# Kernel optimization log

Hardware: AMD Instinct MI355X
Metric: run time of the kernel (lower is better)

The kernel has to match this reference:

```python
import jax, jax.numpy as jnp
import numpy as np

D = 512; NH = 8; FF = 2048; LE = 6; LD = 6; V = 97; SM = 512; SQ = 128; B = 16
EPS = 1e-5


def _posenc(length, depth):
    half = depth // 2
    pos = jnp.arange(length, dtype=jnp.float32)[:, None]
    dep = jnp.arange(half, dtype=jnp.float32)[None, :] / half
    ang = pos / (10000.0 ** dep)
    return jnp.concatenate([jnp.sin(ang), jnp.cos(ang)], axis=-1)  # [length, depth]


def _ln(x, w, b):
    mu = jnp.mean(x, axis=-1, keepdims=True)
    var = jnp.mean((x - mu) ** 2, axis=-1, keepdims=True)
    return (x - mu) * jax.lax.rsqrt(var + EPS) * w + b


def _heads(t, S, Bt):
    return t.reshape(S, Bt * NH, D // NH).transpose(1, 0, 2)  # [B*H, S, dk]


def _self_attn(x, wqkv, bqkv, wo, bo, causal):
    S, Bt, _ = x.shape
    qkv = x @ wqkv.T + bqkv
    q, k, v = jnp.split(qkv, 3, axis=-1)
    q = _heads(q, S, Bt); k = _heads(k, S, Bt); v = _heads(v, S, Bt)
    scores = jnp.einsum('hqd,hkd->hqk', q, k) / jnp.sqrt(jnp.asarray(D // NH, x.dtype))
    if causal:
        mask = jnp.triu(jnp.ones((S, S), bool), 1)
        scores = jnp.where(mask[None], -jnp.inf, scores)
    attn = jax.nn.softmax(scores, axis=-1)
    out = jnp.einsum('hqk,hkd->hqd', attn, v).transpose(1, 0, 2).reshape(S, Bt, D)
    return out @ wo.T + bo


def _cross_attn(query, memory, wq, bq, wk, bk, wv, bv, wo, bo):
    Sq, Bt, _ = query.shape
    Sm = memory.shape[0]
    q = _heads(query @ wq.T + bq, Sq, Bt)
    k = _heads(memory @ wk.T + bk, Sm, Bt)
    v = _heads(memory @ wv.T + bv, Sm, Bt)
    scores = jnp.einsum('hqd,hkd->hqk', q, k) / jnp.sqrt(jnp.asarray(D // NH, query.dtype))
    attn = jax.nn.softmax(scores, axis=-1)
    out = jnp.einsum('hqk,hkd->hqd', attn, v).transpose(1, 0, 2).reshape(Sq, Bt, D)
    return out @ wo.T + bo


def _forward(src, tokens, tok_emb,
             enc_qkv_w, enc_qkv_b, enc_out_w, enc_out_b,
             enc_l1_w, enc_l1_b, enc_l2_w, enc_l2_b,
             enc_n1_w, enc_n1_b, enc_n2_w, enc_n2_b,
             dec_qkv_w, dec_qkv_b, dec_sout_w, dec_sout_b,
             dec_q_w, dec_q_b, dec_k_w, dec_k_b, dec_v_w, dec_v_b,
             dec_cout_w, dec_cout_b,
             dec_l1_w, dec_l1_b, dec_l2_w, dec_l2_b,
             dec_n1_w, dec_n1_b, dec_n2_w, dec_n2_b, dec_n3_w, dec_n3_b,
             out_w, out_b):
    # ---- encoder ----
    x = src  # [SM, B, D]
    for i in range(LE):
        x2 = _self_attn(x, enc_qkv_w[i], enc_qkv_b[i], enc_out_w[i], enc_out_b[i], causal=False)
        x = _ln(x + x2, enc_n1_w[i], enc_n1_b[i])
        x2 = jax.nn.relu(x @ enc_l1_w[i].T + enc_l1_b[i]) @ enc_l2_w[i].T + enc_l2_b[i]
        x = _ln(x + x2, enc_n2_w[i], enc_n2_b[i])
    memory = x
    # ---- decoder ----
    tgt = tok_emb[tokens] + _posenc(tokens.shape[0], D)[:, None, :]  # [SQ, B, D]
    for i in range(LD):
        x2 = _self_attn(tgt, dec_qkv_w[i], dec_qkv_b[i], dec_sout_w[i], dec_sout_b[i], causal=True)
        tgt = _ln(tgt + x2, dec_n1_w[i], dec_n1_b[i])
        x2 = _cross_attn(tgt, memory, dec_q_w[i], dec_q_b[i], dec_k_w[i], dec_k_b[i],
                         dec_v_w[i], dec_v_b[i], dec_cout_w[i], dec_cout_b[i])
        tgt = _ln(tgt + x2, dec_n2_w[i], dec_n2_b[i])
        x2 = jax.nn.relu(tgt @ dec_l1_w[i].T + dec_l1_b[i]) @ dec_l2_w[i].T + dec_l2_b[i]
        tgt = _ln(tgt + x2, dec_n3_w[i], dec_n3_b[i])
    return tgt @ out_w.T + out_b  # [SQ, B, V]


def setup_inputs() -> dict:
    key = jax.random.key(0)
    ks = iter(jax.random.split(key, 64))
    g = lambda shape: jax.random.normal(next(ks), shape, dtype=jnp.float32) * 0.02
    inp = {
        'src': jax.random.normal(next(ks), (SM, B, D), dtype=jnp.float32),
        'tokens': jax.random.randint(next(ks), (SQ, B), 0, V),
        'tok_emb': g((V, D)),
        'enc_qkv_w': g((LE, 3 * D, D)), 'enc_qkv_b': g((LE, 3 * D)),
        'enc_out_w': g((LE, D, D)), 'enc_out_b': g((LE, D)),
        'enc_l1_w': g((LE, FF, D)), 'enc_l1_b': g((LE, FF)),
        'enc_l2_w': g((LE, D, FF)), 'enc_l2_b': g((LE, D)),
        'enc_n1_w': jnp.ones((LE, D)), 'enc_n1_b': jnp.zeros((LE, D)),
        'enc_n2_w': jnp.ones((LE, D)), 'enc_n2_b': jnp.zeros((LE, D)),
        'dec_qkv_w': g((LD, 3 * D, D)), 'dec_qkv_b': g((LD, 3 * D)),
        'dec_sout_w': g((LD, D, D)), 'dec_sout_b': g((LD, D)),
        'dec_q_w': g((LD, D, D)), 'dec_q_b': g((LD, D)),
        'dec_k_w': g((LD, D, D)), 'dec_k_b': g((LD, D)),
        'dec_v_w': g((LD, D, D)), 'dec_v_b': g((LD, D)),
        'dec_cout_w': g((LD, D, D)), 'dec_cout_b': g((LD, D)),
        'dec_l1_w': g((LD, FF, D)), 'dec_l1_b': g((LD, FF)),
        'dec_l2_w': g((LD, D, FF)), 'dec_l2_b': g((LD, D)),
        'dec_n1_w': jnp.ones((LD, D)), 'dec_n1_b': jnp.zeros((LD, D)),
        'dec_n2_w': jnp.ones((LD, D)), 'dec_n2_b': jnp.zeros((LD, D)),
        'dec_n3_w': jnp.ones((LD, D)), 'dec_n3_b': jnp.zeros((LD, D)),
        'out_w': g((V, D)), 'out_b': g((V,)),
    }
    return inp


def reference(src, tokens, tok_emb,
              enc_qkv_w, enc_qkv_b, enc_out_w, enc_out_b,
              enc_l1_w, enc_l1_b, enc_l2_w, enc_l2_b,
              enc_n1_w, enc_n1_b, enc_n2_w, enc_n2_b,
              dec_qkv_w, dec_qkv_b, dec_sout_w, dec_sout_b,
              dec_q_w, dec_q_b, dec_k_w, dec_k_b, dec_v_w, dec_v_b,
              dec_cout_w, dec_cout_b,
              dec_l1_w, dec_l1_b, dec_l2_w, dec_l2_b,
              dec_n1_w, dec_n1_b, dec_n2_w, dec_n2_b, dec_n3_w, dec_n3_b,
              out_w, out_b):
    return _forward(src, tokens, tok_emb,
                    enc_qkv_w, enc_qkv_b, enc_out_w, enc_out_b,
                    enc_l1_w, enc_l1_b, enc_l2_w, enc_l2_b,
                    enc_n1_w, enc_n1_b, enc_n2_w, enc_n2_b,
                    dec_qkv_w, dec_qkv_b, dec_sout_w, dec_sout_b,
                    dec_q_w, dec_q_b, dec_k_w, dec_k_b, dec_v_w, dec_v_b,
                    dec_cout_w, dec_cout_b,
                    dec_l1_w, dec_l1_b, dec_l2_w, dec_l2_b,
                    dec_n1_w, dec_n1_b, dec_n2_w, dec_n2_b, dec_n3_w, dec_n3_b,
                    out_w, out_b)
```

## Files before the change

### kernel.cpp

```cpp
#include <hip/hip_runtime.h>
#include <hip/hip_bf16.h>
#include <cstddef>
#include <cstdint>

#define D_MODEL 512
#define BATCH 16
#define EPS_LN 1e-5f

typedef __bf16 bf16x8 __attribute__((ext_vector_type(8)));
typedef float f32x4 __attribute__((ext_vector_type(4)));
typedef unsigned short u16x8 __attribute__((ext_vector_type(8)));
typedef unsigned short u16x4 __attribute__((ext_vector_type(4)));
typedef unsigned short u16x2 __attribute__((ext_vector_type(2)));

__device__ __forceinline__ void gload_lds16(const void* g, void* l) {
    __builtin_amdgcn_global_load_lds(
        (const __attribute__((address_space(1))) void*)g,
        (__attribute__((address_space(3))) void*)l,
        16, 0, 0);
}

template <int BM, int OUTBF16, int SWAP>
__global__ __launch_bounds__(256) void gemm_mfma(
    const __bf16* __restrict__ A, const __bf16* __restrict__ W,
    const __bf16* __restrict__ W2, int wsplit,
    const float* __restrict__ bias, const float* __restrict__ bias2, int bsplit,
    void* __restrict__ Cout, __bf16* __restrict__ VTout, int m_vt0, int log2S,
    int N, int Mlim, int MS, int K, int relu, int permrow)
{
    constexpr int WC     = (BM == 128) ? 2 : 4;
    constexpr int WSPAN  = 128 / WC;
    constexpr int NC     = WSPAN / 16;
    constexpr int ABYTES = BM * 128;
    constexpr int PA     = ABYTES / 4096;
    constexpr int BUFB   = ABYTES + 16384;

    __shared__ __align__(16) char smem[2 * BUFB];

    const int tid  = threadIdx.x;
    const int lane = tid & 63;
    const int wid  = tid >> 6;
    const int wrow = (BM == 128) ? (wid >> 1) : 0;
    const int wcol = (BM == 128) ? (wid & 1) : wid;
    const int row0 = blockIdx.y * BM;
    const int col0 = blockIdx.x * 128;

    const int lrow  = lane & 15;
    const int lhalf = lane >> 4;
    const int koff0 = ((lhalf) ^ (lrow & 7)) * 16;
    const int koff1 = ((4 + lhalf) ^ (lrow & 7)) * 16;

    const int srow = tid >> 3;
    const int slot = tid & 7;
    const int sg   = slot ^ (srow & 7);

    f32x4 acc[4][NC] = {};

    const __bf16* Wsel = W;
    int wc0 = col0;
    if (col0 >= wsplit) { Wsel = W2; wc0 = col0 - wsplit; }

    const __bf16* Abase = A + (size_t)(row0 + srow) * K + sg * 8;
    const __bf16* Wbase = Wsel + (size_t)(wc0 + srow) * K + sg * 8;

    auto stage = [&](char* buf, int kt) {
#pragma unroll
        for (int p = 0; p < PA; ++p)
            gload_lds16(Abase + (size_t)p * 32 * K + kt, buf + p * 4096 + tid * 16);
#pragma unroll
        for (int p = 0; p < 4; ++p)
            gload_lds16(Wbase + (size_t)p * 32 * K + kt,
                        buf + ABYTES + p * 4096 + tid * 16);
    };

    stage(smem, 0);
    const int nkt = K >> 6;
    int cur = 0;
    for (int kt = 0; kt < nkt; ++kt) {
        __syncthreads();
        if (kt + 1 < nkt) stage(smem + (cur ^ 1) * BUFB, (kt + 1) * 64);
        const char* aB = smem + cur * BUFB + (wrow * 64 + lrow) * 128;
        const char* wB = smem + cur * BUFB + ABYTES + (wcol * WSPAN + lrow) * 128;
#pragma unroll
        for (int ks = 0; ks < 2; ++ks) {
            const int ko = ks ? koff1 : koff0;
            bf16x8 af[4], bfr[NC];
#pragma unroll
            for (int m = 0; m < 4; ++m) af[m]  = *(const bf16x8*)(aB + m * 2048 + ko);
#pragma unroll
            for (int n = 0; n < NC; ++n) bfr[n] = *(const bf16x8*)(wB + n * 2048 + ko);
            if (SWAP) {
#pragma unroll
                for (int m = 0; m < 4; ++m)
#pragma unroll
                    for (int n = 0; n < NC; ++n)
                        acc[m][n] = __builtin_amdgcn_mfma_f32_16x16x32_bf16(
                            bfr[n], af[m], acc[m][n], 0, 0, 0);
            } else {
#pragma unroll
                for (int m = 0; m < 4; ++m)
#pragma unroll
                    for (int n = 0; n < NC; ++n)
                        acc[m][n] = __builtin_amdgcn_mfma_f32_16x16x32_bf16(
                            af[m], bfr[n], acc[m][n], 0, 0, 0);
            }
        }
        cur ^= 1;
    }

    if (SWAP) {
#pragma unroll
        for (int m = 0; m < 4; ++m) {
            const int r = row0 + wrow * 64 + m * 16 + lrow;
#pragma unroll
            for (int n = 0; n < NC; ++n) {
                const int c0 = col0 + wcol * WSPAN + n * 16 + lhalf * 4;
                const float4 bv = *(const float4*)(bias + c0);
                float o0 = acc[m][n][0] + bv.x, o1 = acc[m][n][1] + bv.y;
                float o2 = acc[m][n][2] + bv.z, o3 = acc[m][n][3] + bv.w;
                if (relu) {
                    o0 = fmaxf(o0, 0.f); o1 = fmaxf(o1, 0.f);
                    o2 = fmaxf(o2, 0.f); o3 = fmaxf(o3, 0.f);
                }
                if (OUTBF16) {
                    union { __bf16 h4[4]; u16x4 u; } pk;
                    pk.h4[0] = (__bf16)o0; pk.h4[1] = (__bf16)o1;
                    pk.h4[2] = (__bf16)o2; pk.h4[3] = (__bf16)o3;
                    *(u16x4*)((__bf16*)Cout + (size_t)r * MS + c0) = pk.u;
                } else {
                    *(float4*)((float*)Cout + (size_t)r * MS + c0) =
                        make_float4(o0, o1, o2, o3);
                }
            }
        }
    } else {
        const int orow = row0 + wrow * 64 + lhalf * 4;
        const int ocol = col0 + wcol * WSPAN + lrow;
        const int smask = (1 << log2S) - 1;
#pragma unroll
        for (int n = 0; n < NC; ++n) {
            const int c = ocol + n * 16;
            if (c >= m_vt0) {
                const int cv = c - m_vt0;
                const int hh = cv >> 6, dd = cv & 63;
                const float bv = (bias2 && c >= bsplit) ? bias2[c - bsplit] : bias[c];
#pragma unroll
                for (int m = 0; m < 4; ++m) {
                    const int rr = orow + m * 16;
                    const int bb = rr >> log2S, ss = rr & smask;
                    union { __bf16 h4[4]; u16x4 u; } pk;
#pragma unroll
                    for (int j = 0; j < 4; ++j)
                        pk.h4[j] = (__bf16)(acc[m][n][j] + bv);
                    *(u16x4*)(VTout + (((size_t)((bb * 8 + hh) * 64 + dd)) << log2S) + ss) = pk.u;
                }
            } else if (c < Mlim) {
                const float bv = (bias2 && c >= bsplit) ? bias2[c - bsplit] : bias[c];
#pragma unroll
                for (int m = 0; m < 4; ++m) {
#pragma unroll
                    for (int j = 0; j < 4; ++j) {
                        int rr = orow + m * 16 + j;
                        if (permrow) rr = ((rr & smask) * BATCH) + (rr >> log2S);
                        float v = acc[m][n][j] + bv;
                        if (relu) v = fmaxf(v, 0.f);
                        if (OUTBF16) ((__bf16*)Cout)[(size_t)rr * MS + c] = (__bf16)v;
                        else         ((float*)Cout)[(size_t)rr * MS + c] = v;
                    }
                }
            }
        }
    }
}

template <int CAUSAL>
__global__ __launch_bounds__(256) void attn_mfma(
    const __bf16* __restrict__ Qb, const __bf16* __restrict__ Kb,
    const __bf16* __restrict__ VT, __bf16* __restrict__ Op,
    int Sq, int Skv, int qstride, int kstride, int koff, float scale)
{
    __shared__ __align__(16) char smem[40960];
    const int tid = threadIdx.x;
    const int l   = tid & 63;
    const int w   = tid >> 6;
    char* Psm = smem + 32768 + w * 2048;

    const int qc = blockIdx.x;
    const int h  = blockIdx.y;
    const int b  = blockIdx.z;
    const int l15 = l & 15;
    const int g   = l >> 4;
    const int sw  = l15 & 7;

    const int sq = qc * 64 + w * 16 + l15;
    const __bf16* qrow = Qb + ((size_t)(b * Sq + sq)) * qstride + h * 64 + g * 8;
    const bf16x8 qf0 = *(const bf16x8*)(qrow);
    const bf16x8 qf1 = *(const bf16x8*)(qrow + 32);

    const int srow = tid >> 3;
    const int slot = tid & 7;

    auto stageKV = [&](char* buf, int kc) {
#pragma unroll
        for (int p = 0; p < 2; ++p) {
            const int r   = p * 32 + srow;
            const int sgo = (slot ^ (r & 7)) * 8;
            const __bf16* ksrc = Kb + ((size_t)(b * Skv + kc * 64 + r)) * kstride
                                    + koff + h * 64 + sgo;
            gload_lds16(ksrc, buf + (p * 256 + tid) * 16);
            const __bf16* vsrc = VT + ((size_t)((b * 8 + h) * 64 + r)) * Skv
                                    + kc * 64 + sgo;
            gload_lds16(vsrc, buf + 8192 + (p * 256 + tid) * 16);
        }
    };

    f32x4 acc[4] = {};
    float m_run = -1e30f, l_run = 0.f;

    const int nkc = CAUSAL ? (qc + 1) : (Skv >> 6);
    stageKV(smem, 0);
    int cur = 0;
    for (int kc = 0; kc < nkc; ++kc) {
        __syncthreads();
        if (kc + 1 < nkc) stageKV(smem + (cur ^ 1) * 16384, kc + 1);
        const char* Ksm = smem + cur * 16384;
        const char* Vsm = Ksm + 8192;

        f32x4 st[4];
#pragma unroll
        for (int f = 0; f < 4; ++f) {
            const char* kr = Ksm + (f * 16 + l15) * 128;
            bf16x8 ka0 = *(const bf16x8*)(kr + ((g ^ sw) * 16));
            bf16x8 ka1 = *(const bf16x8*)(kr + (((4 + g) ^ sw) * 16));
            f32x4 z = {};
            z = __builtin_amdgcn_mfma_f32_16x16x32_bf16(ka0, qf0, z, 0, 0, 0);
            st[f] = __builtin_amdgcn_mfma_f32_16x16x32_bf16(ka1, qf1, z, 0, 0, 0);
        }

        float rmax = -1e30f;
#pragma unroll
        for (int f = 0; f < 4; ++f)
#pragma unroll
            for (int j = 0; j < 4; ++j) {
                float v = st[f][j] * scale;
                if (CAUSAL) {
                    if (kc * 64 + f * 16 + g * 4 + j > sq) v = -1e30f;
                }
                st[f][j] = v;
                rmax = fmaxf(rmax, v);
            }
        rmax = fmaxf(rmax, __shfl_xor(rmax, 16, 64));
        rmax = fmaxf(rmax, __shfl_xor(rmax, 32, 64));
        const float mn = fmaxf(m_run, rmax);
        const float corr = __expf(m_run - mn);
        m_run = mn;
        float rsum = 0.f;
#pragma unroll
        for (int f = 0; f < 4; ++f)
#pragma unroll
            for (int j = 0; j < 4; ++j) {
                float p = __expf(st[f][j] - mn);
                st[f][j] = p;
                rsum += p;
            }
        rsum += __shfl_xor(rsum, 16, 64);
        rsum += __shfl_xor(rsum, 32, 64);
        l_run = l_run * corr + rsum;

#pragma unroll
        for (int j = 0; j < 4; ++j) {
            const float cj = __shfl(corr, g * 20 + j, 64);
            acc[0][j] *= cj; acc[1][j] *= cj; acc[2][j] *= cj; acc[3][j] *= cj;
        }

#pragma unroll
        for (int f = 0; f < 4; ++f)
#pragma unroll
            for (int j2 = 0; j2 < 2; ++j2) {
                union { __bf16 h2[2]; unsigned u; } cv;
                cv.h2[0] = (__bf16)st[f][2 * j2];
                cv.h2[1] = (__bf16)st[f][2 * j2 + 1];
                const int key0 = 16 * f + 4 * g + 2 * j2;
                const int byte = l15 * 128 + (((key0 >> 3) ^ sw) * 16) + (key0 & 7) * 2;
                *(unsigned*)(Psm + byte) = cv.u;
            }

#pragma unroll
        for (int ks = 0; ks < 2; ++ks) {
            const int so = ((4 * ks + g) ^ sw) * 16;
            bf16x8 pa = *(const bf16x8*)(Psm + l15 * 128 + so);
#pragma unroll
            for (int n = 0; n < 4; ++n) {
                bf16x8 vb = *(const bf16x8*)(Vsm + (n * 16 + l15) * 128 + so);
                acc[n] = __builtin_amdgcn_mfma_f32_16x16x32_bf16(pa, vb, acc[n], 0, 0, 0);
            }
        }
        cur ^= 1;
    }

    const float inv = 1.f / l_run;
#pragma unroll
    for (int j = 0; j < 4; ++j) {
        const float ij = __shfl(inv, g * 20 + j, 64);
        const int s = qc * 64 + w * 16 + g * 4 + j;
        __bf16* orow = Op + ((size_t)(b * Sq + s)) * D_MODEL + h * 64 + l15;
#pragma unroll
        for (int n = 0; n < 4; ++n)
            orow[n * 16] = (__bf16)(acc[n][j] * ij);
    }
}

__global__ __launch_bounds__(256) void add_ln(
    const float* __restrict__ X, const __bf16* __restrict__ Y,
    const float* __restrict__ w, const float* __restrict__ bias,
    float* __restrict__ Of, __bf16* __restrict__ Oh)
{
    const int t   = blockIdx.x;
    const int tid = threadIdx.x;
    const float2 x2 = *(const float2*)(X + (size_t)t * D_MODEL + tid * 2);
    const u16x2 yv = *(const u16x2*)(Y + (size_t)t * D_MODEL + tid * 2);
    union { u16x2 u; __bf16 h2[2]; } yc; yc.u = yv;
    float v0 = x2.x + (float)yc.h2[0], v1 = x2.y + (float)yc.h2[1];
    float sum = v0 + v1;
    float sq  = v0 * v0 + v1 * v1;
#pragma unroll
    for (int off = 32; off; off >>= 1) {
        sum += __shfl_xor(sum, off);
        sq  += __shfl_xor(sq, off);
    }
    __shared__ float ssum[4], ssq[4];
    const int wid = tid >> 6;
    if ((tid & 63) == 0) { ssum[wid] = sum; ssq[wid] = sq; }
    __syncthreads();
    sum = ssum[0] + ssum[1] + ssum[2] + ssum[3];
    sq  = ssq[0] + ssq[1] + ssq[2] + ssq[3];

    const float mu  = sum * (1.f / D_MODEL);
    const float var = sq * (1.f / D_MODEL) - mu * mu;
    const float rs  = rsqrtf(var + EPS_LN);
    const float2 w2 = *(const float2*)(w + tid * 2);
    const float2 b2 = *(const float2*)(bias + tid * 2);
    float o0 = (v0 - mu) * rs * w2.x + b2.x;
    float o1 = (v1 - mu) * rs * w2.y + b2.y;
    *(float2*)(Of + (size_t)t * D_MODEL + tid * 2) = make_float2(o0, o1);
    union { __bf16 h2[2]; u16x2 u; } cv;
    cv.h2[0] = (__bf16)o0; cv.h2[1] = (__bf16)o1;
    *(u16x2*)(Oh + (size_t)t * D_MODEL + tid * 2) = cv.u;
}

__global__ __launch_bounds__(256) void permute_src(
    const float* __restrict__ src, float* __restrict__ Of, __bf16* __restrict__ Oh)
{
    const int t = blockIdx.x;
    const int b = t >> 9, s = t & 511;
    const int tid = threadIdx.x;
    const float2 v = *(const float2*)(src + ((size_t)(s * BATCH + b)) * D_MODEL + tid * 2);
    *(float2*)(Of + (size_t)t * D_MODEL + tid * 2) = v;
    union { __bf16 h2[2]; u16x2 u; } cv;
    cv.h2[0] = (__bf16)v.x; cv.h2[1] = (__bf16)v.y;
    *(u16x2*)(Oh + (size_t)t * D_MODEL + tid * 2) = cv.u;
}

__global__ __launch_bounds__(256) void embed_pos(
    const int* __restrict__ tokens, const float* __restrict__ emb,
    float* __restrict__ Of, __bf16* __restrict__ Oh)
{
    const int t   = blockIdx.x;
    const int b   = t >> 7, s = t & 127;
    const int tid = threadIdx.x;
    const int tok = tokens[s * BATCH + b];
    const float C = 9.210340371976184f / 256.f;
    const int d = tid * 2;
    const int j = (d < 256) ? d : (d - 256);
    float a0 = (float)s * expf(-(float)j * C);
    float a1 = (float)s * expf(-(float)(j + 1) * C);
    float pe0 = (d < 256) ? sinf(a0) : cosf(a0);
    float pe1 = (d < 256) ? sinf(a1) : cosf(a1);
    const float2 e2 = *(const float2*)(emb + (size_t)tok * D_MODEL + d);
    float o0 = e2.x + pe0, o1 = e2.y + pe1;
    *(float2*)(Of + (size_t)t * D_MODEL + d) = make_float2(o0, o1);
    union { __bf16 h2[2]; u16x2 u; } cv;
    cv.h2[0] = (__bf16)o0; cv.h2[1] = (__bf16)o1;
    *(u16x2*)(Oh + (size_t)t * D_MODEL + d) = cv.u;
}

struct CvtSeg { const float* s; __bf16* d; int n8; };
struct CvtArgs { CvtSeg seg[12]; int tot8; };

__global__ __launch_bounds__(256) void cvt_multi(CvtArgs a)
{
    const int stride = gridDim.x * 256;
    for (int u = blockIdx.x * 256 + threadIdx.x; u < a.tot8; u += stride) {
        int v = u;
        for (int sgi = 0; sgi < 12; ++sgi) {
            const int n8 = a.seg[sgi].n8;
            if (v < n8) {
                const float4 f0 = ((const float4*)a.seg[sgi].s)[v * 2];
                const float4 f1 = ((const float4*)a.seg[sgi].s)[v * 2 + 1];
                union { __bf16 h[8]; u16x8 u; } c;
                c.h[0] = (__bf16)f0.x; c.h[1] = (__bf16)f0.y;
                c.h[2] = (__bf16)f0.z; c.h[3] = (__bf16)f0.w;
                c.h[4] = (__bf16)f1.x; c.h[5] = (__bf16)f1.y;
                c.h[6] = (__bf16)f1.z; c.h[7] = (__bf16)f1.w;
                ((u16x8*)a.seg[sgi].d)[v] = c.u;
                break;
            }
            v -= n8;
        }
    }
}

__global__ __launch_bounds__(256) void pad_outw(
    const float* __restrict__ w, __bf16* __restrict__ o)
{
    const int idx = blockIdx.x * 256 + threadIdx.x;
    const int r = idx >> 9;
    const int c = idx & 511;
    o[idx] = (__bf16)(r < 97 ? w[r * 512 + c] : 0.f);
}

extern "C" void kernel_launch(void* const* d_in, const int* in_sizes, int n_in,
                              void* d_out, int out_size, void* d_ws, size_t ws_size,
                              hipStream_t stream)
{
    const float* src     = (const float*)d_in[0];
    const int*   tokens  = (const int*)d_in[1];
    const float* tok_emb = (const float*)d_in[2];
    const float* enc_qkv_w = (const float*)d_in[3];
    const float* enc_qkv_b = (const float*)d_in[4];
    const float* enc_out_w = (const float*)d_in[5];
    const float* enc_out_b = (const float*)d_in[6];
    const float* enc_l1_w  = (const float*)d_in[7];
    const float* enc_l1_b  = (const float*)d_in[8];
    const float* enc_l2_w  = (const float*)d_in[9];
    const float* enc_l2_b  = (const float*)d_in[10];
    const float* enc_n1_w  = (const float*)d_in[11];
    const float* enc_n1_b  = (const float*)d_in[12];
    const float* enc_n2_w  = (const float*)d_in[13];
    const float* enc_n2_b  = (const float*)d_in[14];
    const float* dec_qkv_w = (const float*)d_in[15];
    const float* dec_qkv_b = (const float*)d_in[16];
    const float* dec_sout_w = (const float*)d_in[17];
    const float* dec_sout_b = (const float*)d_in[18];
    const float* dec_q_w   = (const float*)d_in[19];
    const float* dec_q_b   = (const float*)d_in[20];
    const float* dec_k_w   = (const float*)d_in[21];
    const float* dec_k_b   = (const float*)d_in[22];
    const float* dec_v_w   = (const float*)d_in[23];
    const float* dec_v_b   = (const float*)d_in[24];
    const float* dec_cout_w = (const float*)d_in[25];
    const float* dec_cout_b = (const float*)d_in[26];
    const float* dec_l1_w  = (const float*)d_in[27];
    const float* dec_l1_b  = (const float*)d_in[28];
    const float* dec_l2_w  = (const float*)d_in[29];
    const float* dec_l2_b  = (const float*)d_in[30];
    const float* dec_n1_w  = (const float*)d_in[31];
    const float* dec_n1_b  = (const float*)d_in[32];
    const float* dec_n2_w  = (const float*)d_in[33];
    const float* dec_n2_b  = (const float*)d_in[34];
    const float* dec_n3_w  = (const float*)d_in[35];
    const float* dec_n3_b  = (const float*)d_in[36];
    const float* out_w     = (const float*)d_in[37];
    const float* out_b     = (const float*)d_in[38];

    const int NE = 512 * BATCH;
    const int ND = 128 * BATCH;
    const float scale = 0.125f;
    const int BIG = 1 << 30;

    char* w8 = (char*)d_ws;
    float*  Ax_f = (float*) (w8 + 0);
    float*  T_f  = (float*) (w8 + 16777216);
    __bf16* Ax_h = (__bf16*)(w8 + 20971520);
    __bf16* T_h  = (__bf16*)(w8 + 29360128);
    __bf16* AO_h = (__bf16*)(w8 + 31457280);
    __bf16* Y_h  = (__bf16*)(w8 + 39845888);
    __bf16* VT   = (__bf16*)(w8 + 48234496);
    __bf16* OWp  = (__bf16*)(w8 + 56623104);
    char*   Gb   = w8 + 56754176;
    __bf16* Gqk  = (__bf16*)Gb;
    __bf16* Gh   = (__bf16*)Gb;
    __bf16* Gq   = (__bf16*)Gb;
    __bf16* Gk   = (__bf16*)(Gb + 2097152);
    __bf16* WB   = (__bf16*)(w8 + 90308608);

    const bool upfront = ws_size >= (size_t)178388992;

    auto gemmS = [&](const __bf16* Am, const __bf16* Wm, const float* bv,
                     void* C, int N, int M, int K, int relu) {
        const int nb128 = (M / 128) * (N / 128);
        if (nb128 >= 256) {
            dim3 grid(M / 128, N / 128);
            gemm_mfma<128, 1, 1><<<grid, 256, 0, stream>>>(
                Am, Wm, nullptr, BIG, bv, nullptr, 0, C, nullptr, BIG, 0,
                N, M, M, K, relu, 0);
        } else {
            dim3 grid(M / 128, N / 64);
            gemm_mfma<64, 1, 1><<<grid, 256, 0, stream>>>(
                Am, Wm, nullptr, BIG, bv, nullptr, 0, C, nullptr, BIG, 0,
                N, M, M, K, relu, 0);
        }
    };
    auto gemmN = [&](const __bf16* Am, const __bf16* Wm, const __bf16* W2m, int wsplit,
                     const float* bv, const float* bv2, int bsplit,
                     void* C, __bf16* VTp, int m_vt0, int log2S,
                     int N, int M, int MS, int K, bool outbf, int permrow) {
        const int nb128 = ((M + 127) / 128) * (N / 128);
        if (nb128 >= 256) {
            dim3 grid((M + 127) / 128, N / 128);
            if (outbf) gemm_mfma<128, 1, 0><<<grid, 256, 0, stream>>>(
                Am, Wm, W2m, wsplit, bv, bv2, bsplit, C, VTp, m_vt0, log2S,
                N, M, MS, K, 0, permrow);
            else       gemm_mfma<128, 0, 0><<<grid, 256, 0, stream>>>(
                Am, Wm, W2m, wsplit, bv, bv2, bsplit, C, VTp, m_vt0, log2S,
                N, M, MS, K, 0, permrow);
        } else {
            dim3 grid((M + 127) / 128, N / 64);
            if (outbf) gemm_mfma<64, 1, 0><<<grid, 256, 0, stream>>>(
                Am, Wm, W2m, wsplit, bv, bv2, bsplit, C, VTp, m_vt0, log2S,
                N, M, MS, K, 0, permrow);
            else       gemm_mfma<64, 0, 0><<<grid, 256, 0, stream>>>(
                Am, Wm, W2m, wsplit, bv, bv2, bsplit, C, VTp, m_vt0, log2S,
                N, M, MS, K, 0, permrow);
        }
    };
    auto cvt = [&](CvtArgs& a, int blocks) {
        int tot = 0;
        for (int i = 0; i < 12; ++i) tot += a.seg[i].n8;
        a.tot8 = tot;
        cvt_multi<<<blocks, 256, 0, stream>>>(a);
    };

    permute_src<<<NE, 256, 0, stream>>>(src, Ax_f, Ax_h);
    pad_outw<<<256, 256, 0, stream>>>(out_w, OWp);

    __bf16* WencQKV = WB;
    __bf16* WencOUT = WencQKV + 4718592;
    __bf16* WencL1  = WencOUT + 1572864;
    __bf16* WencL2  = WencL1 + 6291456;
    __bf16* WdecQKV = WencL2 + 6291456;
    __bf16* WdecSOUT = WdecQKV + 4718592;
    __bf16* WdecQ   = WdecSOUT + 1572864;
    __bf16* WdecK   = WdecQ + 1572864;
    __bf16* WdecV   = WdecK + 1572864;
    __bf16* WdecCOUT = WdecV + 1572864;
    __bf16* WdecL1  = WdecCOUT + 1572864;
    __bf16* WdecL2  = WdecL1 + 6291456;

    if (upfront) {
        CvtArgs a = {};
        a.seg[0]  = { enc_qkv_w,  WencQKV,  4718592 / 8 };
        a.seg[1]  = { enc_out_w,  WencOUT,  1572864 / 8 };
        a.seg[2]  = { enc_l1_w,   WencL1,   6291456 / 8 };
        a.seg[3]  = { enc_l2_w,   WencL2,   6291456 / 8 };
        a.seg[4]  = { dec_qkv_w,  WdecQKV,  4718592 / 8 };
        a.seg[5]  = { dec_sout_w, WdecSOUT, 1572864 / 8 };
        a.seg[6]  = { dec_q_w,    WdecQ,    1572864 / 8 };
        a.seg[7]  = { dec_k_w,    WdecK,    1572864 / 8 };
        a.seg[8]  = { dec_v_w,    WdecV,    1572864 / 8 };
        a.seg[9]  = { dec_cout_w, WdecCOUT, 1572864 / 8 };
        a.seg[10] = { dec_l1_w,   WdecL1,   6291456 / 8 };
        a.seg[11] = { dec_l2_w,   WdecL2,   6291456 / 8 };
        cvt(a, 2048);
    }

    for (int i = 0; i < 6; ++i) {
        __bf16 *wqkv, *wout, *wl1, *wl2;
        if (upfront) {
            wqkv = WencQKV + (size_t)i * 786432;
            wout = WencOUT + (size_t)i * 262144;
            wl1  = WencL1 + (size_t)i * 1048576;
            wl2  = WencL2 + (size_t)i * 1048576;
        } else {
            wqkv = WB; wout = WB + 786432; wl1 = WB + 1048576; wl2 = WB + 2097152;
            CvtArgs a = {};
            a.seg[0] = { enc_qkv_w + (size_t)i * 786432,  wqkv, 786432 / 8 };
            a.seg[1] = { enc_out_w + (size_t)i * 262144,  wout, 262144 / 8 };
            a.seg[2] = { enc_l1_w  + (size_t)i * 1048576, wl1, 1048576 / 8 };
            a.seg[3] = { enc_l2_w  + (size_t)i * 1048576, wl2, 1048576 / 8 };
            cvt(a, 1024);
        }

        gemmN(Ax_h, wqkv, nullptr, BIG, enc_qkv_b + (size_t)i * 1536, nullptr, 0,
              Gqk, VT, 1024, 9, NE, 1536, 1024, 512, true, 0);
        attn_mfma<0><<<dim3(8, 8, BATCH), 256, 0, stream>>>(
            Gqk, Gqk, VT, AO_h, 512, 512, 1024, 1024, 512, scale);
        gemmS(AO_h, wout, enc_out_b + (size_t)i * 512, Y_h, NE, 512, 512, 0);
        add_ln<<<NE, 256, 0, stream>>>(Ax_f, Y_h,
                                       enc_n1_w + (size_t)i * 512, enc_n1_b + (size_t)i * 512,
                                       Ax_f, Ax_h);
        gemmS(Ax_h, wl1, enc_l1_b + (size_t)i * 2048, Gh, NE, 2048, 512, 1);
        gemmS(Gh, wl2, enc_l2_b + (size_t)i * 512, Y_h, NE, 512, 2048, 0);
        add_ln<<<NE, 256, 0, stream>>>(Ax_f, Y_h,
                                       enc_n2_w + (size_t)i * 512, enc_n2_b + (size_t)i * 512,
                                       Ax_f, Ax_h);
    }

    embed_pos<<<ND, 256, 0, stream>>>(tokens, tok_emb, T_f, T_h);
    for (int i = 0; i < 6; ++i) {
        __bf16 *dqkv, *dsout, *dq, *dk, *dv, *dcout, *dl1, *dl2;
        if (upfront) {
            dqkv  = WdecQKV + (size_t)i * 786432;
            dsout = WdecSOUT + (size_t)i * 262144;
            dq    = WdecQ + (size_t)i * 262144;
            dk    = WdecK + (size_t)i * 262144;
            dv    = WdecV + (size_t)i * 262144;
            dcout = WdecCOUT + (size_t)i * 262144;
            dl1   = WdecL1 + (size_t)i * 1048576;
            dl2   = WdecL2 + (size_t)i * 1048576;
        } else {
            dqkv = WB; dsout = WB + 786432; dq = WB + 1048576; dk = WB + 1310720;
            dv = WB + 1572864; dcout = WB + 1835008; dl1 = WB + 2097152; dl2 = WB + 3145728;
            CvtArgs a = {};
            a.seg[0] = { dec_qkv_w  + (size_t)i * 786432,  dqkv,  786432 / 8 };
            a.seg[1] = { dec_sout_w + (size_t)i * 262144,  dsout, 262144 / 8 };
            a.seg[2] = { dec_q_w    + (size_t)i * 262144,  dq,    262144 / 8 };
            a.seg[3] = { dec_k_w    + (size_t)i * 262144,  dk,    262144 / 8 };
            a.seg[4] = { dec_v_w    + (size_t)i * 262144,  dv,    262144 / 8 };
            a.seg[5] = { dec_cout_w + (size_t)i * 262144,  dcout, 262144 / 8 };
            a.seg[6] = { dec_l1_w   + (size_t)i * 1048576, dl1,  1048576 / 8 };
            a.seg[7] = { dec_l2_w   + (size_t)i * 1048576, dl2,  1048576 / 8 };
            cvt(a, 1024);
        }

        gemmN(T_h, dqkv, nullptr, BIG, dec_qkv_b + (size_t)i * 1536, nullptr, 0,
              Gqk, VT, 1024, 7, ND, 1536, 1024, 512, true, 0);
        attn_mfma<1><<<dim3(2, 8, BATCH), 256, 0, stream>>>(
            Gqk, Gqk, VT, AO_h, 128, 128, 1024, 1024, 512, scale);
        gemmS(AO_h, dsout, dec_sout_b + (size_t)i * 512, Y_h, ND, 512, 512, 0);
        add_ln<<<ND, 256, 0, stream>>>(T_f, Y_h,
                                       dec_n1_w + (size_t)i * 512, dec_n1_b + (size_t)i * 512,
                                       T_f, T_h);
        gemmS(T_h, dq, dec_q_b + (size_t)i * 512, Gq, ND, 512, 512, 0);
        gemmN(Ax_h, dk, dv, 512, dec_k_b + (size_t)i * 512, dec_v_b + (size_t)i * 512, 512,
              Gk, VT, 512, 9, NE, 1024, 512, 512, true, 0);
        attn_mfma<0><<<dim3(2, 8, BATCH), 256, 0, stream>>>(
            Gq, Gk, VT, AO_h, 128, 512, 512, 512, 0, scale);
        gemmS(AO_h, dcout, dec_cout_b + (size_t)i * 512, Y_h, ND, 512, 512, 0);
        add_ln<<<ND, 256, 0, stream>>>(T_f, Y_h,
                                       dec_n2_w + (size_t)i * 512, dec_n2_b + (size_t)i * 512,
                                       T_f, T_h);
        gemmS(T_h, dl1, dec_l1_b + (size_t)i * 2048, Gh, ND, 2048, 512, 1);
        gemmS(Gh, dl2, dec_l2_b + (size_t)i * 512, Y_h, ND, 512, 2048, 0);
        add_ln<<<ND, 256, 0, stream>>>(T_f, Y_h,
                                       dec_n3_w + (size_t)i * 512, dec_n3_b + (size_t)i * 512,
                                       T_f, T_h);
    }

    gemmN(T_h, OWp, nullptr, BIG, out_b, nullptr, 0,
          (float*)d_out, nullptr, BIG, 7, ND, 97, 97, 512, false, 1);
}
```

Measured before the change: 1.652 ms.

## Use 512-thread GEMM blocks with 8 waves and simplify weight conversion segment lookup

```diff
diff --git a/kernel.cpp b/kernel.cpp
--- a/kernel.cpp
+++ b/kernel.cpp
@@ -21,18 +21,17 @@
 }
 
 template <int BM, int OUTBF16, int SWAP>
-__global__ __launch_bounds__(256) void gemm_mfma(
+__global__ __launch_bounds__(512) void gemm_mfma(
     const __bf16* __restrict__ A, const __bf16* __restrict__ W,
     const __bf16* __restrict__ W2, int wsplit,
     const float* __restrict__ bias, const float* __restrict__ bias2, int bsplit,
     void* __restrict__ Cout, __bf16* __restrict__ VTout, int m_vt0, int log2S,
     int N, int Mlim, int MS, int K, int relu, int permrow)
 {
-    constexpr int WC     = (BM == 128) ? 2 : 4;
-    constexpr int WSPAN  = 128 / WC;
-    constexpr int NC     = WSPAN / 16;
+    constexpr int MR     = BM / 32;
+    constexpr int WRSPAN = BM / 2;
     constexpr int ABYTES = BM * 128;
-    constexpr int PA     = ABYTES / 4096;
+    constexpr int PA     = ABYTES / 8192;
     constexpr int BUFB   = ABYTES + 16384;
 
     __shared__ __align__(16) char smem[2 * BUFB];
@@ -40,8 +39,8 @@
     const int tid  = threadIdx.x;
     const int lane = tid & 63;
     const int wid  = tid >> 6;
-    const int wrow = (BM == 128) ? (wid >> 1) : 0;
-    const int wcol = (BM == 128) ? (wid & 1) : wid;
+    const int wrow = wid >> 2;
+    const int wcol = wid & 3;
     const int row0 = blockIdx.y * BM;
     const int col0 = blockIdx.x * 128;
 
@@ -54,7 +53,7 @@
     const int slot = tid & 7;
     const int sg   = slot ^ (srow & 7);
 
-    f32x4 acc[4][NC] = {};
+    f32x4 acc[MR][2] = {};
 
     const __bf16* Wsel = W;
     int wc0 = col0;
@@ -66,11 +65,11 @@
     auto stage = [&](char* buf, int kt) {
 #pragma unroll
         for (int p = 0; p < PA; ++p)
-            gload_lds16(Abase + (size_t)p * 32 * K + kt, buf + p * 4096 + tid * 16);
-#pragma unroll
-        for (int p = 0; p < 4; ++p)
-            gload_lds16(Wbase + (size_t)p * 32 * K + kt,
-                        buf + ABYTES + p * 4096 + tid * 16);
+            gload_lds16(Abase + (size_t)p * 64 * K + kt, buf + p * 8192 + tid * 16);
+#pragma unroll
+        for (int p = 0; p < 2; ++p)
+            gload_lds16(Wbase + (size_t)p * 64 * K + kt,
+                        buf + ABYTES + p * 8192 + tid * 16);
     };
 
     stage(smem, 0);
@@ -79,28 +78,28 @@
     for (int kt = 0; kt < nkt; ++kt) {
         __syncthreads();
         if (kt + 1 < nkt) stage(smem + (cur ^ 1) * BUFB, (kt + 1) * 64);
-        const char* aB = smem + cur * BUFB + (wrow * 64 + lrow) * 128;
-        const char* wB = smem + cur * BUFB + ABYTES + (wcol * WSPAN + lrow) * 128;
+        const char* aB = smem + cur * BUFB + (wrow * WRSPAN + lrow) * 128;
+        const char* wB = smem + cur * BUFB + ABYTES + (wcol * 32 + lrow) * 128;
 #pragma unroll
         for (int ks = 0; ks < 2; ++ks) {
             const int ko = ks ? koff1 : koff0;
-            bf16x8 af[4], bfr[NC];
-#pragma unroll
-            for (int m = 0; m < 4; ++m) af[m]  = *(const bf16x8*)(aB + m * 2048 + ko);
-#pragma unroll
-            for (int n = 0; n < NC; ++n) bfr[n] = *(const bf16x8*)(wB + n * 2048 + ko);
+            bf16x8 af[MR], bfr[2];
+#pragma unroll
+            for (int m = 0; m < MR; ++m) af[m]  = *(const bf16x8*)(aB + m * 2048 + ko);
+#pragma unroll
+            for (int n = 0; n < 2; ++n)  bfr[n] = *(const bf16x8*)(wB + n * 2048 + ko);
             if (SWAP) {
 #pragma unroll
-                for (int m = 0; m < 4; ++m)
-#pragma unroll
-                    for (int n = 0; n < NC; ++n)
+                for (int m = 0; m < MR; ++m)
+#pragma unroll
+                    for (int n = 0; n < 2; ++n)
                         acc[m][n] = __builtin_amdgcn_mfma_f32_16x16x32_bf16(
                             bfr[n], af[m], acc[m][n], 0, 0, 0);
             } else {
 #pragma unroll
-                for (int m = 0; m < 4; ++m)
-#pragma unroll
-                    for (int n = 0; n < NC; ++n)
+                for (int m = 0; m < MR; ++m)
+#pragma unroll
+                    for (int n = 0; n < 2; ++n)
                         acc[m][n] = __builtin_amdgcn_mfma_f32_16x16x32_bf16(
                             af[m], bfr[n], acc[m][n], 0, 0, 0);
             }
@@ -110,11 +109,11 @@
 
     if (SWAP) {
 #pragma unroll
-        for (int m = 0; m < 4; ++m) {
-            const int r = row0 + wrow * 64 + m * 16 + lrow;
-#pragma unroll
-            for (int n = 0; n < NC; ++n) {
-                const int c0 = col0 + wcol * WSPAN + n * 16 + lhalf * 4;
+        for (int m = 0; m < MR; ++m) {
+            const int r = row0 + wrow * WRSPAN + m * 16 + lrow;
+#pragma unroll
+            for (int n = 0; n < 2; ++n) {
+                const int c0 = col0 + wcol * 32 + n * 16 + lhalf * 4;
                 const float4 bv = *(const float4*)(bias + c0);
                 float o0 = acc[m][n][0] + bv.x, o1 = acc[m][n][1] + bv.y;
                 float o2 = acc[m][n][2] + bv.z, o3 = acc[m][n][3] + bv.w;
@@ -134,18 +133,18 @@
             }
         }
     } else {
-        const int orow = row0 + wrow * 64 + lhalf * 4;
-        const int ocol = col0 + wcol * WSPAN + lrow;
+        const int orow = row0 + wrow * WRSPAN + lhalf * 4;
+        const int ocol = col0 + wcol * 32 + lrow;
         const int smask = (1 << log2S) - 1;
 #pragma unroll
-        for (int n = 0; n < NC; ++n) {
+        for (int n = 0; n < 2; ++n) {
             const int c = ocol + n * 16;
             if (c >= m_vt0) {
                 const int cv = c - m_vt0;
                 const int hh = cv >> 6, dd = cv & 63;
                 const float bv = (bias2 && c >= bsplit) ? bias2[c - bsplit] : bias[c];
 #pragma unroll
-                for (int m = 0; m < 4; ++m) {
+                for (int m = 0; m < MR; ++m) {
                     const int rr = orow + m * 16;
                     const int bb = rr >> log2S, ss = rr & smask;
                     union { __bf16 h4[4]; u16x4 u; } pk;
@@ -157,7 +156,7 @@
             } else if (c < Mlim) {
                 const float bv = (bias2 && c >= bsplit) ? bias2[c - bsplit] : bias[c];
 #pragma unroll
-                for (int m = 0; m < 4; ++m) {
+                for (int m = 0; m < MR; ++m) {
 #pragma unroll
                     for (int j = 0; j < 4; ++j) {
                         int rr = orow + m * 16 + j;
@@ -390,23 +389,19 @@
 __global__ __launch_bounds__(256) void cvt_multi(CvtArgs a)
 {
     const int stride = gridDim.x * 256;
+    int sgi = 0;
+    int base = 0;
     for (int u = blockIdx.x * 256 + threadIdx.x; u < a.tot8; u += stride) {
-        int v = u;
-        for (int sgi = 0; sgi < 12; ++sgi) {
-            const int n8 = a.seg[sgi].n8;
-            if (v < n8) {
-                const float4 f0 = ((const float4*)a.seg[sgi].s)[v * 2];
-                const float4 f1 = ((const float4*)a.seg[sgi].s)[v * 2 + 1];
-                union { __bf16 h[8]; u16x8 u; } c;
-                c.h[0] = (__bf16)f0.x; c.h[1] = (__bf16)f0.y;
-                c.h[2] = (__bf16)f0.z; c.h[3] = (__bf16)f0.w;
-                c.h[4] = (__bf16)f1.x; c.h[5] = (__bf16)f1.y;
-                c.h[6] = (__bf16)f1.z; c.h[7] = (__bf16)f1.w;
-                ((u16x8*)a.seg[sgi].d)[v] = c.u;
-                break;
-            }
-            v -= n8;
-        }
+        while (u - base >= a.seg[sgi].n8) { base += a.seg[sgi].n8; ++sgi; }
+        const int v = u - base;
+        const float4 f0 = ((const float4*)a.seg[sgi].s)[v * 2];
+        const float4 f1 = ((const float4*)a.seg[sgi].s)[v * 2 + 1];
+        union { __bf16 h[8]; u16x8 u; } c;
+        c.h[0] = (__bf16)f0.x; c.h[1] = (__bf16)f0.y;
+        c.h[2] = (__bf16)f0.z; c.h[3] = (__bf16)f0.w;
+        c.h[4] = (__bf16)f1.x; c.h[5] = (__bf16)f1.y;
+        c.h[6] = (__bf16)f1.z; c.h[7] = (__bf16)f1.w;
+        ((u16x8*)a.seg[sgi].d)[v] = c.u;
     }
 }
 
@@ -489,14 +484,14 @@
     auto gemmS = [&](const __bf16* Am, const __bf16* Wm, const float* bv,
                      void* C, int N, int M, int K, int relu) {
         const int nb128 = (M / 128) * (N / 128);
-        if (nb128 >= 256) {
+        if (nb128 >= 512) {
             dim3 grid(M / 128, N / 128);
-            gemm_mfma<128, 1, 1><<<grid, 256, 0, stream>>>(
+            gemm_mfma<128, 1, 1><<<grid, 512, 0, stream>>>(
                 Am, Wm, nullptr, BIG, bv, nullptr, 0, C, nullptr, BIG, 0,
                 N, M, M, K, relu, 0);
         } else {
             dim3 grid(M / 128, N / 64);
-            gemm_mfma<64, 1, 1><<<grid, 256, 0, stream>>>(
+            gemm_mfma<64, 1, 1><<<grid, 512, 0, stream>>>(
                 Am, Wm, nullptr, BIG, bv, nullptr, 0, C, nullptr, BIG, 0,
                 N, M, M, K, relu, 0);
         }
@@ -506,20 +501,20 @@
                      void* C, __bf16* VTp, int m_vt0, int log2S,
                      int N, int M, int MS, int K, bool outbf, int permrow) {
         const int nb128 = ((M + 127) / 128) * (N / 128);
-        if (nb128 >= 256) {
+        if (nb128 >= 512) {
             dim3 grid((M + 127) / 128, N / 128);
-            if (outbf) gemm_mfma<128, 1, 0><<<grid, 256, 0, stream>>>(
+            if (outbf) gemm_mfma<128, 1, 0><<<grid, 512, 0, stream>>>(
                 Am, Wm, W2m, wsplit, bv, bv2, bsplit, C, VTp, m_vt0, log2S,
                 N, M, MS, K, 0, permrow);
-            else       gemm_mfma<128, 0, 0><<<grid, 256, 0, stream>>>(
+            else       gemm_mfma<128, 0, 0><<<grid, 512, 0, stream>>>(
                 Am, Wm, W2m, wsplit, bv, bv2, bsplit, C, VTp, m_vt0, log2S,
                 N, M, MS, K, 0, permrow);
         } else {
             dim3 grid((M + 127) / 128, N / 64);
-            if (outbf) gemm_mfma<64, 1, 0><<<grid, 256, 0, stream>>>(
+            if (outbf) gemm_mfma<64, 1, 0><<<grid, 512, 0, stream>>>(
                 Am, Wm, W2m, wsplit, bv, bv2, bsplit, C, VTp, m_vt0, log2S,
                 N, M, MS, K, 0, permrow);
-            else       gemm_mfma<64, 0, 0><<<grid, 256, 0, stream>>>(
+            else       gemm_mfma<64, 0, 0><<<grid, 512, 0, stream>>>(
                 Am, Wm, W2m, wsplit, bv, bv2, bsplit, C, VTp, m_vt0, log2S,
                 N, M, MS, K, 0, permrow);
         }
@@ -561,7 +556,7 @@
         a.seg[9]  = { dec_cout_w, WdecCOUT, 1572864 / 8 };
         a.seg[10] = { dec_l1_w,   WdecL1,   6291456 / 8 };
         a.seg[11] = { dec_l2_w,   WdecL2,   6291456 / 8 };
-        cvt(a, 2048);
+        cvt(a, 4096);
     }
 
     for (int i = 0; i < 6; ++i) {
```

New measurement: 1.534 ms. 1.08x faster.
